# Kernel optimization log

Hardware: AMD Instinct MI355X
Metric: run time of the kernel (lower is better)

Reference implementation:

```python
import jax, jax.numpy as jnp
import numpy as np

T, B, E, H = 2048, 2, 1024, 16
Dh = E // H


def setup_inputs() -> dict:
    key = jax.random.key(0)
    ks = jax.random.split(key, 5)
    s = 0.02
    query = jax.random.normal(ks[0], (T, B, E), dtype=jnp.float32)
    Wq = jax.random.normal(ks[1], (E, E), dtype=jnp.float32) * s
    Wk = jax.random.normal(ks[2], (E, E), dtype=jnp.float32) * s
    Wv = jax.random.normal(ks[3], (E, E), dtype=jnp.float32) * s
    Wo = jax.random.normal(ks[4], (E, E), dtype=jnp.float32) * s
    bq = jnp.zeros((E,), jnp.float32)
    bk = jnp.zeros((E,), jnp.float32)
    bv = jnp.zeros((E,), jnp.float32)
    bo = jnp.zeros((E,), jnp.float32)
    # additive causal mask: 0 on/below diagonal, -inf above (standard fairseq usage)
    neg = jnp.finfo(jnp.float32).min
    attn_mask = jnp.where(jnp.triu(jnp.ones((T, T), jnp.bool_), k=1), neg, 0.0).astype(jnp.float32)
    return {"query": query, "Wq": Wq, "bq": bq, "Wk": Wk, "bk": bk,
            "Wv": Wv, "bv": bv, "Wo": Wo, "bo": bo, "attn_mask": attn_mask}


def reference(query, Wq, bq, Wk, bk, Wv, bv, Wo, bo, attn_mask):
    t, b, e = query.shape
    scale = Dh ** -0.5
    # self-attention projections (nn.Linear: x @ W.T + b)
    q = (query @ Wq.T + bq) * scale  # [T,B,E]
    k = query @ Wk.T + bk
    v = query @ Wv.T + bv
    # [T, B*H, Dh] -> [B*H, T, Dh]
    q = q.reshape(t, b * H, Dh).transpose(1, 0, 2)
    k = k.reshape(t, b * H, Dh).transpose(1, 0, 2)
    v = v.reshape(t, b * H, Dh).transpose(1, 0, 2)
    # explicit bmm -> softmax -> bmm (materializes [B*H, T, T])
    attn_weights = jnp.einsum('btd,bsd->bts', q, k) + attn_mask[None, :, :]
    attn_probs = jax.nn.softmax(attn_weights, axis=-1)
    attn = jnp.einsum('bts,bsd->btd', attn_probs, v)  # [B*H, T, Dh]
    attn = attn.transpose(1, 0, 2).reshape(t, b, e)  # [T,B,E]
    out = attn @ Wo.T + bo
    return out
```

## Files before the change

kernel.cpp:

```cpp
#include <hip/hip_runtime.h>


typedef __attribute__((ext_vector_type(8))) short   s16x8;
typedef __attribute__((ext_vector_type(4))) float   f32x4;
typedef __attribute__((ext_vector_type(2))) __fp16  f16x2;
typedef __attribute__((ext_vector_type(4))) __fp16  f16x4;

#define MFMA16(a, b, c) __builtin_amdgcn_mfma_f32_16x16x32_bf16((a), (b), (c), 0, 0, 0)
#define MFMApv(a, b, c) __builtin_amdgcn_mfma_f32_16x16x16f16((a), (b), (c), 0, 0, 0)

static __device__ __forceinline__ unsigned short f2bf(float f) {
    unsigned u = __float_as_uint(f);
    unsigned r = u + 0x7fffu + ((u >> 16) & 1u);
    return (unsigned short)(r >> 16);
}

static __device__ __forceinline__ void gl2lds16(const void* g, void* l) {
    __builtin_amdgcn_global_load_lds(
        (const __attribute__((address_space(1))) unsigned int*)g,
        (__attribute__((address_space(3))) unsigned int*)l, 16, 0, 0);
}

__global__ __launch_bounds__(256) void cvt_x(const float* __restrict__ src,
                                             unsigned short* __restrict__ dst,
                                             int n4) {
    int i = blockIdx.x * 256 + threadIdx.x;
    if (i < n4) {
        const float4 f = reinterpret_cast<const float4*>(src)[i];
        ushort4 u;
        u.x = f2bf(f.x); u.y = f2bf(f.y); u.z = f2bf(f.z); u.w = f2bf(f.w);
        reinterpret_cast<ushort4*>(dst)[i] = u;
    }
}

__global__ __launch_bounds__(256) void cvt_w4(const float* __restrict__ w0,
                                              const float* __restrict__ w1,
                                              const float* __restrict__ w2,
                                              const float* __restrict__ w3,
                                              unsigned short* __restrict__ dst) {
    const int blk = blockIdx.x;
    const int sel = blk >> 10;
    const int i   = (blk & 1023) * 256 + threadIdx.x;
    const float* src = (sel == 0) ? w0 : (sel == 1) ? w1 : (sel == 2) ? w2 : w3;
    const float4 f = reinterpret_cast<const float4*>(src)[i];
    ushort4 u;
    u.x = f2bf(f.x); u.y = f2bf(f.y); u.z = f2bf(f.z); u.w = f2bf(f.w);
    reinterpret_cast<ushort4*>(dst + (size_t)sel * 1048576)[i] = u;
}

__global__ __launch_bounds__(256) void gemm128(const unsigned short* __restrict__ A,
                                               const unsigned short* __restrict__ W,
                                               const float* __restrict__ b0,
                                               const float* __restrict__ b1,
                                               const float* __restrict__ b2,
                                               unsigned short* __restrict__ outB,
                                               float* __restrict__ outF,
                                               int qkv) {
    __shared__ unsigned short Al[128 * 32];
    __shared__ unsigned short Bl[128 * 32];

    const int tid  = threadIdx.x;
    const int w    = tid >> 6;
    const int lane = tid & 63;
    const int quad = lane >> 4;
    const int c    = lane & 15;
    const int wm   = w >> 1;
    const int wn   = w & 1;

    const int m0 = blockIdx.y * 128;
    const int n0 = blockIdx.x * 128;

    f32x4 acc[4][4];
    #pragma unroll
    for (int mi = 0; mi < 4; ++mi)
        #pragma unroll
        for (int ni = 0; ni < 4; ++ni) acc[mi][ni] = (f32x4){0.f, 0.f, 0.f, 0.f};

    const int srow = tid >> 2;
    const int sci  = (tid & 3) ^ ((tid >> 3) & 3);
    const unsigned short* aG = A + (size_t)(m0 + srow) * 1024 + sci * 8;
    const unsigned short* wG = W + (size_t)(n0 + srow) * 1024 + sci * 8;
    unsigned short* aL = &Al[srow * 32 + (tid & 3) * 8];
    unsigned short* wL = &Bl[srow * 32 + (tid & 3) * 8];

    const int swz = (quad ^ ((c >> 1) & 3)) * 8;

    for (int kk = 0; kk < 32; ++kk) {
        const int k0 = kk * 32;
        __syncthreads();
        gl2lds16(aG + k0,              aL);
        gl2lds16(aG + k0 + 64 * 1024,  aL + 64 * 32);
        gl2lds16(wG + k0,              wL);
        gl2lds16(wG + k0 + 64 * 1024,  wL + 64 * 32);
        __syncthreads();

        s16x8 af[4], bf[4];
        #pragma unroll
        for (int mi = 0; mi < 4; ++mi)
            af[mi] = *reinterpret_cast<const s16x8*>(&Al[(wm * 64 + mi * 16 + c) * 32 + swz]);
        #pragma unroll
        for (int ni = 0; ni < 4; ++ni)
            bf[ni] = *reinterpret_cast<const s16x8*>(&Bl[(wn * 64 + ni * 16 + c) * 32 + swz]);
        #pragma unroll
        for (int mi = 0; mi < 4; ++mi)
            #pragma unroll
            for (int ni = 0; ni < 4; ++ni)
                acc[mi][ni] = MFMA16(af[mi], bf[ni], acc[mi][ni]);
    }

    if (qkv) {
        #pragma unroll
        for (int ni = 0; ni < 4; ++ni) {
            const int n   = n0 + wn * 64 + ni * 16 + c;
            const int sel = n >> 10;
            const float* bias = (sel == 0) ? b0 : (sel == 1) ? b1 : b2;
            const float bval  = bias[n & 1023];
            const float scale = (sel == 0) ? 0.18033688011112042f : 1.0f;
            #pragma unroll
            for (int mi = 0; mi < 4; ++mi)
                #pragma unroll
                for (int r = 0; r < 4; ++r) {
                    const int m = m0 + wm * 64 + mi * 16 + quad * 4 + r;
                    outB[(size_t)m * 3072 + n] = f2bf((acc[mi][ni][r] + bval) * scale);
                }
        }
    } else {
        #pragma unroll
        for (int ni = 0; ni < 4; ++ni) {
            const int n = n0 + wn * 64 + ni * 16 + c;
            const float bval = b0[n];
            #pragma unroll
            for (int mi = 0; mi < 4; ++mi)
                #pragma unroll
                for (int r = 0; r < 4; ++r) {
                    const int m = m0 + wm * 64 + mi * 16 + quad * 4 + r;
                    outF[(size_t)m * 1024 + n] = acc[mi][ni][r] + bval;
                }
        }
    }
}

__global__ __launch_bounds__(256) void vtrans(const unsigned short* __restrict__ QKV,
                                              __fp16* __restrict__ Vt) {
    __shared__ unsigned short tile[64][66];
    const int tid = threadIdx.x;
    const int bh = blockIdx.x, b = bh >> 4, h = bh & 15;
    const int tt0 = blockIdx.y * 64;

    #pragma unroll
    for (int round = 0; round < 2; ++round) {
        const int idx = round * 256 + tid;
        const int tl = idx >> 3, dc = idx & 7;
        const s16x8 v = *reinterpret_cast<const s16x8*>(
            QKV + (size_t)(2 * (tt0 + tl) + b) * 3072 + 2048 + h * 64 + dc * 8);
        union { s16x8 s; unsigned int u[4]; } uu; uu.s = v;
        unsigned int* tp = (unsigned int*)&tile[tl][dc * 8];
        tp[0] = uu.u[0]; tp[1] = uu.u[1]; tp[2] = uu.u[2]; tp[3] = uu.u[3];
    }
    __syncthreads();

    #pragma unroll
    for (int round = 0; round < 2; ++round) {
        const int idx = round * 256 + tid;
        const int d = idx >> 3, tch = (idx & 7) * 8;
        union { uint4 u4; unsigned int u[4]; } o;
        #pragma unroll
        for (int k = 0; k < 4; ++k) {
            const float f0 = __uint_as_float((unsigned)tile[tch + 2 * k][d] << 16);
            const float f1 = __uint_as_float((unsigned)tile[tch + 2 * k + 1][d] << 16);
            const f16x2 hh = __builtin_amdgcn_cvt_pkrtz(f0, f1);
            o.u[k] = __builtin_bit_cast(unsigned int, hh);
        }
        *reinterpret_cast<uint4*>(Vt + ((size_t)bh * 64 + d) * 2048 + tt0 + tch) = o.u4;
    }
}

__global__ __launch_bounds__(256, 2) void attn_kernel(const unsigned short* __restrict__ QKV,
                                                      const __fp16* __restrict__ Vt,
                                                      unsigned short* __restrict__ Ob) {
    __shared__ unsigned short Kl[2][64][32];
    __shared__ __fp16 Vl[64][72];

    const int tid  = threadIdx.x;
    const int w    = tid >> 6;
    const int lane = tid & 63;
    const int quad = lane >> 4;
    const int c    = lane & 15;

    const int bh = blockIdx.x, bB = bh >> 4, h = bh & 15;
    const int p  = blockIdx.y;
    const int aT[2]   = { 31 - p, p };
    const int trgT[2] = { aT[0] * 64 + w * 16, aT[1] * 64 + w * 16 };
    const int nIt = 32 - p;

    s16x8 aq[2][2];
    #pragma unroll
    for (int t = 0; t < 2; ++t) {
        const unsigned short* qp = QKV + (size_t)(2 * (trgT[t] + c) + bB) * 3072 + h * 64 + quad * 8;
        aq[t][0] = *reinterpret_cast<const s16x8*>(qp);
        aq[t][1] = *reinterpret_cast<const s16x8*>(qp + 32);
    }

    const int lr  = lane >> 2;
    const int lci = (lane & 3) ^ ((lane >> 3) & 3);
    const unsigned short* kSrc = QKV + (size_t)(2 * (w * 16 + lr) + bB) * 3072
                                 + 1024 + h * 64 + lci * 8;
    unsigned short* kDst0 = &Kl[0][w * 16 + lr][(lane & 3) * 8];
    unsigned short* kDst1 = &Kl[1][w * 16 + lr][(lane & 3) * 8];

    const int vr = tid >> 3, vci = tid & 7;
    const __fp16* vSrc = Vt + ((size_t)bh * 64 + vr) * 2048 + vci * 8;
    __fp16* vDst0 = &Vl[vr][vci * 8];
    __fp16* vDst1 = &Vl[vr + 32][vci * 8];

    f32x4 acc[2][4];
    float l[2] = {0.f, 0.f};
    #pragma unroll
    for (int t = 0; t < 2; ++t)
        #pragma unroll
        for (int dt = 0; dt < 4; ++dt) acc[t][dt] = (f32x4){0.f, 0.f, 0.f, 0.f};

    const int swz = (quad ^ ((c >> 1) & 3)) * 8;

    for (int it = 0; it < nIt; ++it) {
        const int s0 = it * 64;
        __syncthreads();
        const uint4 va = *reinterpret_cast<const uint4*>(vSrc + s0);
        const uint4 vb = *reinterpret_cast<const uint4*>(vSrc + 32 * 2048 + s0);
        gl2lds16(kSrc + (size_t)s0 * 6144,      kDst0);
        gl2lds16(kSrc + (size_t)s0 * 6144 + 32, kDst1);
        *reinterpret_cast<uint4*>(vDst0) = va;
        *reinterpret_cast<uint4*>(vDst1) = vb;
        __syncthreads();

        s16x8 kf[4][2];
        #pragma unroll
        for (int ns = 0; ns < 4; ++ns) {
            kf[ns][0] = *reinterpret_cast<const s16x8*>(&Kl[0][ns * 16 + c][swz]);
            kf[ns][1] = *reinterpret_cast<const s16x8*>(&Kl[1][ns * 16 + c][swz]);
        }
        f16x4 vf[4][4];
        #pragma unroll
        for (int dt = 0; dt < 4; ++dt)
            #pragma unroll
            for (int ch = 0; ch < 4; ++ch)
                vf[dt][ch] = *reinterpret_cast<const f16x4*>(&Vl[dt * 16 + c][ch * 16 + quad * 4]);

        #pragma unroll
        for (int t = 0; t < 2; ++t) {
            if (it > aT[t]) continue;
            const bool diag = (it == aT[t]);
            f32x4 sT[4];
            #pragma unroll
            for (int ns = 0; ns < 4; ++ns) {
                f32x4 z = (f32x4){0.f, 0.f, 0.f, 0.f};
                z = MFMA16(kf[ns][0], aq[t][0], z);
                sT[ns] = MFMA16(kf[ns][1], aq[t][1], z);
            }
            f16x4 pf[4];
            float lp = 0.f;
            #pragma unroll
            for (int ns = 0; ns < 4; ++ns) {
                float pv[4];
                #pragma unroll
                for (int r = 0; r < 4; ++r) pv[r] = exp2f(sT[ns][r]);
                if (diag) {
                    const int sb = s0 + ns * 16 + quad * 4;
                    const int qg = trgT[t] + c;
                    #pragma unroll
                    for (int r = 0; r < 4; ++r) if (sb + r > qg) pv[r] = 0.f;
                }
                lp += (pv[0] + pv[1]) + (pv[2] + pv[3]);
                const f16x2 lo = __builtin_amdgcn_cvt_pkrtz(pv[0], pv[1]);
                const f16x2 hi = __builtin_amdgcn_cvt_pkrtz(pv[2], pv[3]);
                pf[ns] = __builtin_shufflevector(lo, hi, 0, 1, 2, 3);
            }
            l[t] += lp;
            #pragma unroll
            for (int dt = 0; dt < 4; ++dt)
                #pragma unroll
                for (int ns = 0; ns < 4; ++ns)
                    acc[t][dt] = MFMApv(vf[dt][ns], pf[ns], acc[t][dt]);
        }
    }

    #pragma unroll
    for (int t = 0; t < 2; ++t) {
        float lv = l[t];
        lv += __shfl_xor(lv, 16);
        lv += __shfl_xor(lv, 32);
        const float inv = 1.0f / lv;
        const size_t base = (size_t)(2 * (trgT[t] + c) + bB) * 1024 + h * 64;
        #pragma unroll
        for (int dt = 0; dt < 4; ++dt) {
            const unsigned u0 = (unsigned)f2bf(acc[t][dt][0] * inv)
                              | ((unsigned)f2bf(acc[t][dt][1] * inv) << 16);
            const unsigned u1 = (unsigned)f2bf(acc[t][dt][2] * inv)
                              | ((unsigned)f2bf(acc[t][dt][3] * inv) << 16);
            uint2 st; st.x = u0; st.y = u1;
            *reinterpret_cast<uint2*>(Ob + base + dt * 16 + quad * 4) = st;
        }
    }
}

extern "C" void kernel_launch(void* const* d_in, const int* in_sizes, int n_in,
                              void* d_out, int out_size, void* d_ws, size_t ws_size,
                              hipStream_t stream) {
    const float* query = (const float*)d_in[0];
    const float* Wq    = (const float*)d_in[1];
    const float* bq    = (const float*)d_in[2];
    const float* Wk    = (const float*)d_in[3];
    const float* bk    = (const float*)d_in[4];
    const float* Wv    = (const float*)d_in[5];
    const float* bv    = (const float*)d_in[6];
    const float* Wo    = (const float*)d_in[7];
    const float* bo    = (const float*)d_in[8];

    float* out = (float*)d_out;

    unsigned short* ws    = (unsigned short*)d_ws;
    unsigned short* Xbf   = ws;
    unsigned short* Wcat  = Xbf  + (size_t)4096 * 1024;
    unsigned short* QKVb  = Wcat + (size_t)4 * 1024 * 1024;
    __fp16*         Vtw   = (__fp16*)(QKVb + (size_t)4096 * 3072);
    unsigned short* attnb = (unsigned short*)(Vtw + (size_t)32 * 64 * 2048);

    cvt_x<<<4096, 256, 0, stream>>>(query, Xbf, 4096 * 1024 / 4);
    cvt_w4<<<4096, 256, 0, stream>>>(Wq, Wk, Wv, Wo, Wcat);

    gemm128<<<dim3(24, 32), 256, 0, stream>>>(Xbf, Wcat, bq, bk, bv,
                                              QKVb, nullptr, 1);

    vtrans<<<dim3(32, 32), 256, 0, stream>>>(QKVb, Vtw);

    attn_kernel<<<dim3(32, 16), 256, 0, stream>>>(QKVb, Vtw, attnb);

    gemm128<<<dim3(8, 32), 256, 0, stream>>>(attnb, Wcat + (size_t)3 * 1024 * 1024,
                                             bo, nullptr, nullptr, nullptr, out, 0);
}
```

Measured before the change: 209.9 us.

## Fuse V transpose into QKV GEMM epilogue and double-buffer attention K/V loads

Merges the two fp32-to-bf16 conversion kernels into one launch. It also reorders activation rows to batch-major during conversion, so Q/K and V land in per-head-friendly layouts. The QKV GEMM epilogue now writes V directly as transposed fp16, which removes the separate vtrans kernel and its round trip through memory. The attention kernel double-buffers K and V tiles with async global-to-LDS loads and XOR-swizzles V, dropping one barrier per iteration. The costs are scattered V stores, more LDS per block, and a strided final-output store in the output GEMM.

```diff
diff --git a/kernel.cpp b/kernel.cpp
--- a/kernel.cpp
+++ b/kernel.cpp
@@ -21,31 +21,31 @@
         (__attribute__((address_space(3))) unsigned int*)l, 16, 0, 0);
 }
 
-__global__ __launch_bounds__(256) void cvt_x(const float* __restrict__ src,
-                                             unsigned short* __restrict__ dst,
-                                             int n4) {
-    int i = blockIdx.x * 256 + threadIdx.x;
-    if (i < n4) {
+__global__ __launch_bounds__(256) void cvt_all(const float* __restrict__ query,
+                                               const float* __restrict__ w0,
+                                               const float* __restrict__ w1,
+                                               const float* __restrict__ w2,
+                                               const float* __restrict__ w3,
+                                               unsigned short* __restrict__ Xb,
+                                               unsigned short* __restrict__ Wcat) {
+    const int bx = blockIdx.x;
+    if (bx < 4096) {
+        const int i = threadIdx.x;
+        const float4 f = reinterpret_cast<const float4*>(query + (size_t)bx * 1024)[i];
+        ushort4 u;
+        u.x = f2bf(f.x); u.y = f2bf(f.y); u.z = f2bf(f.z); u.w = f2bf(f.w);
+        const int mrow = (bx & 1) * 2048 + (bx >> 1);
+        reinterpret_cast<ushort4*>(Xb + (size_t)mrow * 1024)[i] = u;
+    } else {
+        const int j   = bx - 4096;
+        const int sel = j >> 10;
+        const int i   = (j & 1023) * 256 + threadIdx.x;
+        const float* src = (sel == 0) ? w0 : (sel == 1) ? w1 : (sel == 2) ? w2 : w3;
         const float4 f = reinterpret_cast<const float4*>(src)[i];
         ushort4 u;
         u.x = f2bf(f.x); u.y = f2bf(f.y); u.z = f2bf(f.z); u.w = f2bf(f.w);
-        reinterpret_cast<ushort4*>(dst)[i] = u;
-    }
-}
-
-__global__ __launch_bounds__(256) void cvt_w4(const float* __restrict__ w0,
-                                              const float* __restrict__ w1,
-                                              const float* __restrict__ w2,
-                                              const float* __restrict__ w3,
-                                              unsigned short* __restrict__ dst) {
-    const int blk = blockIdx.x;
-    const int sel = blk >> 10;
-    const int i   = (blk & 1023) * 256 + threadIdx.x;
-    const float* src = (sel == 0) ? w0 : (sel == 1) ? w1 : (sel == 2) ? w2 : w3;
-    const float4 f = reinterpret_cast<const float4*>(src)[i];
-    ushort4 u;
-    u.x = f2bf(f.x); u.y = f2bf(f.y); u.z = f2bf(f.z); u.w = f2bf(f.w);
-    reinterpret_cast<ushort4*>(dst + (size_t)sel * 1048576)[i] = u;
+        reinterpret_cast<ushort4*>(Wcat + (size_t)sel * 1048576)[i] = u;
+    }
 }
 
 __global__ __launch_bounds__(256) void gemm128(const unsigned short* __restrict__ A,
@@ -53,7 +53,8 @@
                                                const float* __restrict__ b0,
                                                const float* __restrict__ b1,
                                                const float* __restrict__ b2,
-                                               unsigned short* __restrict__ outB,
+                                               unsigned short* __restrict__ outQK,
+                                               __fp16* __restrict__ outV,
                                                float* __restrict__ outF,
                                                int qkv) {
     __shared__ unsigned short Al[128 * 32];
@@ -109,20 +110,42 @@
     }
 
     if (qkv) {
-        #pragma unroll
-        for (int ni = 0; ni < 4; ++ni) {
-            const int n   = n0 + wn * 64 + ni * 16 + c;
-            const int sel = n >> 10;
-            const float* bias = (sel == 0) ? b0 : (sel == 1) ? b1 : b2;
-            const float bval  = bias[n & 1023];
+        const int sel = n0 >> 10;
+        if (sel < 2) {
             const float scale = (sel == 0) ? 0.18033688011112042f : 1.0f;
-            #pragma unroll
-            for (int mi = 0; mi < 4; ++mi)
-                #pragma unroll
-                for (int r = 0; r < 4; ++r) {
-                    const int m = m0 + wm * 64 + mi * 16 + quad * 4 + r;
-                    outB[(size_t)m * 3072 + n] = f2bf((acc[mi][ni][r] + bval) * scale);
+            const float* bias = (sel == 0) ? b0 : b1;
+            #pragma unroll
+            for (int ni = 0; ni < 4; ++ni) {
+                const int n = n0 + wn * 64 + ni * 16 + c;
+                const float bval = bias[n & 1023];
+                #pragma unroll
+                for (int mi = 0; mi < 4; ++mi)
+                    #pragma unroll
+                    for (int r = 0; r < 4; ++r) {
+                        const int m = m0 + wm * 64 + mi * 16 + quad * 4 + r;
+                        outQK[(size_t)m * 2048 + n] = f2bf((acc[mi][ni][r] + bval) * scale);
+                    }
+            }
+        } else {
+            #pragma unroll
+            for (int ni = 0; ni < 4; ++ni) {
+                const int vcol = n0 - 2048 + wn * 64 + ni * 16 + c;
+                const int h = vcol >> 6, d = vcol & 63;
+                const float bval = b2[vcol];
+                #pragma unroll
+                for (int mi = 0; mi < 4; ++mi) {
+                    const int m = m0 + wm * 64 + mi * 16 + quad * 4;
+                    const int bb = m >> 11, t = m & 2047;
+                    const f16x2 lo = __builtin_amdgcn_cvt_pkrtz(acc[mi][ni][0] + bval,
+                                                                acc[mi][ni][1] + bval);
+                    const f16x2 hi = __builtin_amdgcn_cvt_pkrtz(acc[mi][ni][2] + bval,
+                                                                acc[mi][ni][3] + bval);
+                    uint2 st;
+                    st.x = __builtin_bit_cast(unsigned int, lo);
+                    st.y = __builtin_bit_cast(unsigned int, hi);
+                    *reinterpret_cast<uint2*>(outV + ((size_t)((bb * 16 + h) * 64 + d)) * 2048 + t) = st;
                 }
+            }
         }
     } else {
         #pragma unroll
@@ -130,56 +153,22 @@
             const int n = n0 + wn * 64 + ni * 16 + c;
             const float bval = b0[n];
             #pragma unroll
-            for (int mi = 0; mi < 4; ++mi)
-                #pragma unroll
-                for (int r = 0; r < 4; ++r) {
-                    const int m = m0 + wm * 64 + mi * 16 + quad * 4 + r;
-                    outF[(size_t)m * 1024 + n] = acc[mi][ni][r] + bval;
-                }
-        }
-    }
-}
-
-__global__ __launch_bounds__(256) void vtrans(const unsigned short* __restrict__ QKV,
-                                              __fp16* __restrict__ Vt) {
-    __shared__ unsigned short tile[64][66];
-    const int tid = threadIdx.x;
-    const int bh = blockIdx.x, b = bh >> 4, h = bh & 15;
-    const int tt0 = blockIdx.y * 64;
-
-    #pragma unroll
-    for (int round = 0; round < 2; ++round) {
-        const int idx = round * 256 + tid;
-        const int tl = idx >> 3, dc = idx & 7;
-        const s16x8 v = *reinterpret_cast<const s16x8*>(
-            QKV + (size_t)(2 * (tt0 + tl) + b) * 3072 + 2048 + h * 64 + dc * 8);
-        union { s16x8 s; unsigned int u[4]; } uu; uu.s = v;
-        unsigned int* tp = (unsigned int*)&tile[tl][dc * 8];
-        tp[0] = uu.u[0]; tp[1] = uu.u[1]; tp[2] = uu.u[2]; tp[3] = uu.u[3];
-    }
-    __syncthreads();
-
-    #pragma unroll
-    for (int round = 0; round < 2; ++round) {
-        const int idx = round * 256 + tid;
-        const int d = idx >> 3, tch = (idx & 7) * 8;
-        union { uint4 u4; unsigned int u[4]; } o;
-        #pragma unroll
-        for (int k = 0; k < 4; ++k) {
-            const float f0 = __uint_as_float((unsigned)tile[tch + 2 * k][d] << 16);
-            const float f1 = __uint_as_float((unsigned)tile[tch + 2 * k + 1][d] << 16);
-            const f16x2 hh = __builtin_amdgcn_cvt_pkrtz(f0, f1);
-            o.u[k] = __builtin_bit_cast(unsigned int, hh);
-        }
-        *reinterpret_cast<uint4*>(Vt + ((size_t)bh * 64 + d) * 2048 + tt0 + tch) = o.u4;
-    }
-}
-
-__global__ __launch_bounds__(256, 2) void attn_kernel(const unsigned short* __restrict__ QKV,
+            for (int mi = 0; mi < 4; ++mi) {
+                const int m = m0 + wm * 64 + mi * 16 + quad * 4;
+                const int bb = m >> 11, t = m & 2047;
+                #pragma unroll
+                for (int r = 0; r < 4; ++r)
+                    outF[(size_t)(2 * (t + r) + bb) * 1024 + n] = acc[mi][ni][r] + bval;
+            }
+        }
+    }
+}
+
+__global__ __launch_bounds__(256, 2) void attn_kernel(const unsigned short* __restrict__ QKb,
                                                       const __fp16* __restrict__ Vt,
                                                       unsigned short* __restrict__ Ob) {
-    __shared__ unsigned short Kl[2][64][32];
-    __shared__ __fp16 Vl[64][72];
+    __shared__ unsigned short Kl[2][2][64][32];
+    __shared__ __fp16 Vl[2][64][64];
 
     const int tid  = threadIdx.x;
     const int w    = tid >> 6;
@@ -196,22 +185,17 @@
     s16x8 aq[2][2];
     #pragma unroll
     for (int t = 0; t < 2; ++t) {
-        const unsigned short* qp = QKV + (size_t)(2 * (trgT[t] + c) + bB) * 3072 + h * 64 + quad * 8;
+        const unsigned short* qp = QKb + (size_t)(bB * 2048 + trgT[t] + c) * 2048 + h * 64 + quad * 8;
         aq[t][0] = *reinterpret_cast<const s16x8*>(qp);
         aq[t][1] = *reinterpret_cast<const s16x8*>(qp + 32);
     }
 
-    const int lr  = lane >> 2;
-    const int lci = (lane & 3) ^ ((lane >> 3) & 3);
-    const unsigned short* kSrc = QKV + (size_t)(2 * (w * 16 + lr) + bB) * 3072
-                                 + 1024 + h * 64 + lci * 8;
-    unsigned short* kDst0 = &Kl[0][w * 16 + lr][(lane & 3) * 8];
-    unsigned short* kDst1 = &Kl[1][w * 16 + lr][(lane & 3) * 8];
-
-    const int vr = tid >> 3, vci = tid & 7;
-    const __fp16* vSrc = Vt + ((size_t)bh * 64 + vr) * 2048 + vci * 8;
-    __fp16* vDst0 = &Vl[vr][vci * 8];
-    __fp16* vDst1 = &Vl[vr + 32][vci * 8];
+    const int lr4 = lane >> 2, sl4 = lane & 3;
+    const unsigned short* kSrc = QKb + (size_t)(bB * 2048 + w * 16 + lr4) * 2048
+                                 + 1024 + h * 64 + (sl4 ^ ((lane >> 3) & 3)) * 8;
+    const int vr8 = lane >> 3, sl8 = lane & 7;
+    const __fp16* vSrcA = Vt + (size_t)(bh * 64 + w * 16 + vr8) * 2048 + (sl8 ^ vr8) * 8;
+    const __fp16* vSrcB = vSrcA + (size_t)8 * 2048;
 
     f32x4 acc[2][4];
     float l[2] = {0.f, 0.f};
@@ -220,32 +204,43 @@
         #pragma unroll
         for (int dt = 0; dt < 4; ++dt) acc[t][dt] = (f32x4){0.f, 0.f, 0.f, 0.f};
 
-    const int swz = (quad ^ ((c >> 1) & 3)) * 8;
+    const int kswz = (quad ^ ((c >> 1) & 3)) * 8;
+
+    {
+        gl2lds16(kSrc,      &Kl[0][0][w * 16 + lr4][sl4 * 8]);
+        gl2lds16(kSrc + 32, &Kl[0][1][w * 16 + lr4][sl4 * 8]);
+        gl2lds16(vSrcA,     &Vl[0][w * 16 + vr8][sl8 * 8]);
+        gl2lds16(vSrcB,     &Vl[0][w * 16 + 8 + vr8][sl8 * 8]);
+    }
 
     for (int it = 0; it < nIt; ++it) {
+        const int buf = it & 1;
+        __syncthreads();
+        if (it + 1 < nIt) {
+            const size_t s1 = (size_t)(it + 1) * 64;
+            const int nb = buf ^ 1;
+            gl2lds16(kSrc + s1 * 2048,      &Kl[nb][0][w * 16 + lr4][sl4 * 8]);
+            gl2lds16(kSrc + s1 * 2048 + 32, &Kl[nb][1][w * 16 + lr4][sl4 * 8]);
+            gl2lds16(vSrcA + s1,            &Vl[nb][w * 16 + vr8][sl8 * 8]);
+            gl2lds16(vSrcB + s1,            &Vl[nb][w * 16 + 8 + vr8][sl8 * 8]);
+        }
+
+        s16x8 kf[4][2];
+        #pragma unroll
+        for (int ns = 0; ns < 4; ++ns) {
+            kf[ns][0] = *reinterpret_cast<const s16x8*>(&Kl[buf][0][ns * 16 + c][kswz]);
+            kf[ns][1] = *reinterpret_cast<const s16x8*>(&Kl[buf][1][ns * 16 + c][kswz]);
+        }
+        f16x4 vf[4][4];
+        #pragma unroll
+        for (int dt = 0; dt < 4; ++dt)
+            #pragma unroll
+            for (int ch = 0; ch < 4; ++ch) {
+                const int phys = ((2 * ch + (quad >> 1)) ^ (c & 7)) * 8 + (quad & 1) * 4;
+                vf[dt][ch] = *reinterpret_cast<const f16x4*>(&Vl[buf][dt * 16 + c][phys]);
+            }
+
         const int s0 = it * 64;
-        __syncthreads();
-        const uint4 va = *reinterpret_cast<const uint4*>(vSrc + s0);
-        const uint4 vb = *reinterpret_cast<const uint4*>(vSrc + 32 * 2048 + s0);
-        gl2lds16(kSrc + (size_t)s0 * 6144,      kDst0);
-        gl2lds16(kSrc + (size_t)s0 * 6144 + 32, kDst1);
-        *reinterpret_cast<uint4*>(vDst0) = va;
-        *reinterpret_cast<uint4*>(vDst1) = vb;
-        __syncthreads();
-
-        s16x8 kf[4][2];
-        #pragma unroll
-        for (int ns = 0; ns < 4; ++ns) {
-            kf[ns][0] = *reinterpret_cast<const s16x8*>(&Kl[0][ns * 16 + c][swz]);
-            kf[ns][1] = *reinterpret_cast<const s16x8*>(&Kl[1][ns * 16 + c][swz]);
-        }
-        f16x4 vf[4][4];
-        #pragma unroll
-        for (int dt = 0; dt < 4; ++dt)
-            #pragma unroll
-            for (int ch = 0; ch < 4; ++ch)
-                vf[dt][ch] = *reinterpret_cast<const f16x4*>(&Vl[dt * 16 + c][ch * 16 + quad * 4]);
-
         #pragma unroll
         for (int t = 0; t < 2; ++t) {
             if (it > aT[t]) continue;
@@ -290,7 +285,7 @@
         lv += __shfl_xor(lv, 16);
         lv += __shfl_xor(lv, 32);
         const float inv = 1.0f / lv;
-        const size_t base = (size_t)(2 * (trgT[t] + c) + bB) * 1024 + h * 64;
+        const size_t base = (size_t)(bB * 2048 + trgT[t] + c) * 1024 + h * 64;
         #pragma unroll
         for (int dt = 0; dt < 4; ++dt) {
             const unsigned u0 = (unsigned)f2bf(acc[t][dt][0] * inv)
@@ -321,20 +316,17 @@
     unsigned short* ws    = (unsigned short*)d_ws;
     unsigned short* Xbf   = ws;
     unsigned short* Wcat  = Xbf  + (size_t)4096 * 1024;
-    unsigned short* QKVb  = Wcat + (size_t)4 * 1024 * 1024;
-    __fp16*         Vtw   = (__fp16*)(QKVb + (size_t)4096 * 3072);
+    unsigned short* QKb   = Wcat + (size_t)4 * 1024 * 1024;
+    __fp16*         Vtw   = (__fp16*)(QKb + (size_t)4096 * 2048);
     unsigned short* attnb = (unsigned short*)(Vtw + (size_t)32 * 64 * 2048);
 
-    cvt_x<<<4096, 256, 0, stream>>>(query, Xbf, 4096 * 1024 / 4);
-    cvt_w4<<<4096, 256, 0, stream>>>(Wq, Wk, Wv, Wo, Wcat);
+    cvt_all<<<8192, 256, 0, stream>>>(query, Wq, Wk, Wv, Wo, Xbf, Wcat);
 
     gemm128<<<dim3(24, 32), 256, 0, stream>>>(Xbf, Wcat, bq, bk, bv,
-                                              QKVb, nullptr, 1);
-
-    vtrans<<<dim3(32, 32), 256, 0, stream>>>(QKVb, Vtw);
-
-    attn_kernel<<<dim3(32, 16), 256, 0, stream>>>(QKVb, Vtw, attnb);
+                                              QKb, Vtw, nullptr, 1);
+
+    attn_kernel<<<dim3(32, 16), 256, 0, stream>>>(QKb, Vtw, attnb);
 
     gemm128<<<dim3(8, 32), 256, 0, stream>>>(attnb, Wcat + (size_t)3 * 1024 * 1024,
-                                             bo, nullptr, nullptr, nullptr, out, 0);
-}
+                                             bo, nullptr, nullptr, nullptr, nullptr, out, 0);
+}
```

Measured after the change: 217.5 us. 3.6% more time.
